# Kernel optimization log

Hardware: AMD Instinct MI355X
Metric: run time of the kernel (lower is better)

## Reference

```python
import jax, jax.numpy as jnp
import numpy as np

NUM_TOKENS = 8192
CODEBOOK_DIM = 64
BETA = 0.25
DECAY = 0.99
EPS = 1e-05
B, C, H, W = 32, 64, 32, 32


def setup_inputs() -> dict:
    key = jax.random.key(0)
    k1, k2, k3, k4 = jax.random.split(key, 4)
    z = jax.random.normal(k1, (B, C, H, W), dtype=jnp.float32)
    emb = jax.random.normal(k2, (NUM_TOKENS, CODEBOOK_DIM), dtype=jnp.float32)
    ema_w = jax.random.normal(k3, (NUM_TOKENS, CODEBOOK_DIM), dtype=jnp.float32)
    cluster_size = jax.random.uniform(k4, (NUM_TOKENS,), dtype=jnp.float32)
    return {"z": z, "emb": emb, "ema_w": ema_w, "cluster_size": cluster_size}


def reference(z, emb, ema_w, cluster_size):
    # NCHW -> NHWC, flatten to [N, D]
    z_nhwc = jnp.transpose(z, (0, 2, 3, 1))
    z_flat = z_nhwc.reshape(-1, CODEBOOK_DIM)  # [N, D]

    # squared distances: ||z||^2 + ||e||^2 - 2 z e^T  -> [N, K]
    d = (jnp.sum(z_flat * z_flat, axis=1, keepdims=True)
         + jnp.sum(emb * emb, axis=1)
         - 2.0 * jnp.einsum('nd,kd->nk', z_flat, emb))
    idx = jnp.argmin(d, axis=1)  # [N] int

    z_q = emb[idx].reshape(z_nhwc.shape)  # gather + reshape

    # EMA updates (training-mode buffer math); one-hot matmuls expressed as segment sums
    new_cluster = jax.ops.segment_sum(jnp.ones_like(idx, dtype=z.dtype), idx, num_segments=NUM_TOKENS)
    cs = DECAY * cluster_size + (1.0 - DECAY) * new_cluster
    new_ema_w = jax.ops.segment_sum(z_flat, idx, num_segments=NUM_TOKENS)
    ema_w_out = DECAY * ema_w + (1.0 - DECAY) * new_ema_w
    cs_sum = jnp.sum(cs)
    cs_norm = (cs + EPS) / (cs_sum + NUM_TOKENS * EPS)
    emb_out = ema_w_out / cs_norm[:, None]

    # commitment loss uses z_q from the OLD codebook (as in torch code)
    loss = BETA * jnp.mean((jax.lax.stop_gradient(z_q) - z_nhwc) ** 2)

    # straight-through estimator, back to NCHW
    z_q_st = z_nhwc + jax.lax.stop_gradient(z_q - z_nhwc)
    z_q_st = jnp.transpose(z_q_st, (0, 3, 1, 2))
    return z_q_st, loss, idx, cs_norm, ema_w_out, emb_out
```

## Files before the change

kernel.cpp:

```cpp
#include <hip/hip_runtime.h>
#include <float.h>

#define N_TOK   32768
#define DIM     64
#define K_CODES 8192
#define HWSZ    1024
#define CHW     65536
#define NELEM   2097152

typedef short  bf16x8 __attribute__((ext_vector_type(8)));
typedef float  f32x16 __attribute__((ext_vector_type(16)));

static __device__ __forceinline__ unsigned short f2bf(float x) {
    unsigned u = __float_as_uint(x);
    unsigned r = u + 0x7FFFu + ((u >> 16) & 1u);
    return (unsigned short)(r >> 16);
}
static __device__ __forceinline__ float bf2f(unsigned short h) {
    return __uint_as_float(((unsigned)h) << 16);
}

__global__ __launch_bounds__(256) void prep_e(const float* __restrict__ emb,
                                              unsigned short* __restrict__ blob,
                                              float* __restrict__ eng,
                                              unsigned long long* __restrict__ packed,
                                              int* __restrict__ cnt_i,
                                              float* __restrict__ sums) {
    __shared__ float part[512];
    const int gid = blockIdx.x * 256 + threadIdx.x;
    packed[gid] = ~0ull;
    if (gid < K_CODES) cnt_i[gid] = 0;
    if (gid < 2) sums[gid] = 0.f;

    int tile = blockIdx.x;
    #pragma unroll
    for (int u0 = 0; u0 < 2; ++u0) {
        int u = threadIdx.x + u0 * 256;
        int s = u >> 7, h = (u >> 6) & 1, n = u & 63;
        const float* src = emb + (tile * 64 + n) * 64 + s * 16 + h * 8;
        float4 v0 = *(const float4*)src;
        float4 v1 = *(const float4*)(src + 4);
        float x[8] = {v0.x, v0.y, v0.z, v0.w, v1.x, v1.y, v1.z, v1.w};
        unsigned short hi[8], lo[8];
        float ss = 0.f;
        #pragma unroll
        for (int j = 0; j < 8; ++j) {
            hi[j] = f2bf(x[j]);
            lo[j] = f2bf(x[j] - bf2f(hi[j]));
            ss += x[j] * x[j];
        }
        part[u] = ss;
        unsigned short* dhi = blob + (size_t)tile * 8192 + ((s * 2 + 0) * 2 + h) * 512 + n * 8;
        unsigned short* dlo = blob + (size_t)tile * 8192 + ((s * 2 + 1) * 2 + h) * 512 + n * 8;
        uint4 ph, pl;
        ph.x = (unsigned)hi[0] | ((unsigned)hi[1] << 16);
        ph.y = (unsigned)hi[2] | ((unsigned)hi[3] << 16);
        ph.z = (unsigned)hi[4] | ((unsigned)hi[5] << 16);
        ph.w = (unsigned)hi[6] | ((unsigned)hi[7] << 16);
        pl.x = (unsigned)lo[0] | ((unsigned)lo[1] << 16);
        pl.y = (unsigned)lo[2] | ((unsigned)lo[3] << 16);
        pl.z = (unsigned)lo[4] | ((unsigned)lo[5] << 16);
        pl.w = (unsigned)lo[6] | ((unsigned)lo[7] << 16);
        *(uint4*)dhi = ph;
        *(uint4*)dlo = pl;
    }
    __syncthreads();
    if (threadIdx.x < 64) {
        float s = 0.f;
        #pragma unroll
        for (int j = 0; j < 8; ++j) s += part[threadIdx.x + j * 64];
        eng[tile * 64 + threadIdx.x] = s;
    }
}

static __device__ __forceinline__ void loadB(const unsigned short* __restrict__ base,
                                             int h, bf16x8* Bh, bf16x8* Bl) {
    #pragma unroll
    for (int s = 0; s < 4; ++s) {
        Bh[s] = *(const bf16x8*)(base + (4 * s + h) * 512);
        Bl[s] = *(const bf16x8*)(base + (4 * s + 2 + h) * 512);
    }
}

__global__ __launch_bounds__(256, 2) void vq_argmin(const float* __restrict__ z,
                                                    const unsigned short* __restrict__ blob,
                                                    const float* __restrict__ eng,
                                                    unsigned long long* __restrict__ packed) {
    __shared__ __align__(16) unsigned short zh[128 * 72];
    __shared__ __align__(16) unsigned short zl[128 * 72];
    __shared__ unsigned long long red[256];

    const int tid  = threadIdx.x;
    const int lane = tid & 63;
    const int wid  = tid >> 6;
    const int wr   = wid >> 1, wc = wid & 1;
    const int l31  = lane & 31, h = lane >> 5;

    const int tb = blockIdx.x & 255;
    const int ks = blockIdx.x >> 8;
    const int n0 = tb * 128;
    const int zbase = (n0 >> 10) * CHW + (n0 & 1023);
    const int t0 = ks * 64, t1 = t0 + 64;
    const int wcb = (wc * 32 + l31) * 8;
    const int colb = wc * 32 + l31;

    {
        int f4 = tid & 31;
        int c0 = tid >> 5;
        #pragma unroll
        for (int r = 0; r < 8; ++r) {
            int c = c0 * 8 + r;
            float4 v = *(const float4*)(z + zbase + c * HWSZ + f4 * 4);
            float x[4] = {v.x, v.y, v.z, v.w};
            #pragma unroll
            for (int e = 0; e < 4; ++e) {
                int t = f4 * 4 + e;
                unsigned short hi = f2bf(x[e]);
                zh[t * 72 + c] = hi;
                zl[t * 72 + c] = f2bf(x[e] - bf2f(hi));
            }
        }
    }

    bf16x8 B0h[4], B0l[4], B1h[4], B1l[4];
    float engv0, engv1;
    loadB(blob + (size_t)t0 * 8192 + wcb, h, B0h, B0l);
    engv0 = eng[t0 * 64 + colb];

    __syncthreads();

    bf16x8 Af[2][4][2];
    #pragma unroll
    for (int mt = 0; mt < 2; ++mt) {
        int row = wr * 64 + mt * 32 + l31;
        #pragma unroll
        for (int s = 0; s < 4; ++s) {
            Af[mt][s][0] = *(const bf16x8*)(&zh[row * 72 + s * 16 + h * 8]);
            Af[mt][s][1] = *(const bf16x8*)(&zl[row * 72 + s * 16 + h * 8]);
        }
    }

    float minv0[16], minv1[16];
    int   mini0[16], mini1[16];
    #pragma unroll
    for (int r = 0; r < 16; ++r) {
        minv0[r] = FLT_MAX; minv1[r] = FLT_MAX;
        mini0[r] = 0;       mini1[r] = 0;
    }

    #define COMPUTE(KT, BH, BL, ENGV)                                                  \
    {                                                                                  \
        f32x16 ac0, ac1;                                                               \
        _Pragma("unroll")                                                              \
        for (int r = 0; r < 16; ++r) { ac0[r] = 0.f; ac1[r] = 0.f; }                   \
        _Pragma("unroll")                                                              \
        for (int s = 0; s < 4; ++s) {                                                  \
            ac0 = __builtin_amdgcn_mfma_f32_32x32x16_bf16(Af[0][s][1], BH[s], ac0, 0, 0, 0); \
            ac1 = __builtin_amdgcn_mfma_f32_32x32x16_bf16(Af[1][s][1], BH[s], ac1, 0, 0, 0); \
            ac0 = __builtin_amdgcn_mfma_f32_32x32x16_bf16(Af[0][s][0], BL[s], ac0, 0, 0, 0); \
            ac1 = __builtin_amdgcn_mfma_f32_32x32x16_bf16(Af[1][s][0], BL[s], ac1, 0, 0, 0); \
            ac0 = __builtin_amdgcn_mfma_f32_32x32x16_bf16(Af[0][s][0], BH[s], ac0, 0, 0, 0); \
            ac1 = __builtin_amdgcn_mfma_f32_32x32x16_bf16(Af[1][s][0], BH[s], ac1, 0, 0, 0); \
        }                                                                              \
        const int col = (KT) * 64 + colb;                                              \
        _Pragma("unroll")                                                              \
        for (int r = 0; r < 16; ++r) {                                                 \
            float d0 = fmaf(-2.f, ac0[r], ENGV);                                       \
            if (d0 < minv0[r]) { minv0[r] = d0; mini0[r] = col; }                      \
            float d1 = fmaf(-2.f, ac1[r], ENGV);                                       \
            if (d1 < minv1[r]) { minv1[r] = d1; mini1[r] = col; }                      \
        }                                                                              \
    }

    for (int kt = t0; kt < t1; kt += 2) {
        loadB(blob + (size_t)(kt + 1) * 8192 + wcb, h, B1h, B1l);
        engv1 = eng[(kt + 1) * 64 + colb];
        COMPUTE(kt, B0h, B0l, engv0);
        if (kt + 2 < t1) {
            loadB(blob + (size_t)(kt + 2) * 8192 + wcb, h, B0h, B0l);
            engv0 = eng[(kt + 2) * 64 + colb];
        }
        COMPUTE(kt + 1, B1h, B1l, engv1);
    }
    #undef COMPUTE

    #pragma unroll
    for (int mt = 0; mt < 2; ++mt) {
        unsigned long long pv[16];
        #pragma unroll
        for (int r = 0; r < 16; ++r) {
            float v = mt ? minv1[r] : minv0[r];
            int   i = mt ? mini1[r] : mini0[r];
            unsigned u = __float_as_uint(v);
            u = (u & 0x80000000u) ? ~u : (u | 0x80000000u);
            pv[r] = ((unsigned long long)u << 32) | (unsigned)i;
        }
        #pragma unroll
        for (int m = 1; m <= 16; m <<= 1) {
            #pragma unroll
            for (int r = 0; r < 16; ++r) {
                unsigned long long o = __shfl_xor(pv[r], m, 64);
                if (o < pv[r]) pv[r] = o;
            }
        }
        #pragma unroll
        for (int r = 0; r < 16; ++r) {
            if (l31 == r) {
                int row = wr * 64 + mt * 32 + (r & 3) + 8 * (r >> 2) + 4 * h;
                red[row * 2 + wc] = pv[r];
            }
        }
    }
    __syncthreads();
    if (tid < 128) {
        unsigned long long a = red[tid * 2], b = red[tid * 2 + 1];
        unsigned long long m = (b < a) ? b : a;
        atomicMin(&packed[n0 + tid], m);
    }
}

__global__ __launch_bounds__(256) void zq_loss(const float* __restrict__ z,
                                               const float* __restrict__ emb,
                                               const float* __restrict__ ema_w,
                                               const unsigned long long* __restrict__ packed,
                                               float* __restrict__ zq_out,
                                               float* __restrict__ idx_out,
                                               int* __restrict__ idx_i32,
                                               int* __restrict__ cnt_i,
                                               float* __restrict__ loss_sum,
                                               float* __restrict__ z_t,
                                               float* __restrict__ emao_out) {
    const int tid = threadIdx.x;
    const int n0  = blockIdx.x * 64;
    const int t   = tid >> 2, q = tid & 3;
    const int n   = n0 + t;
    const int idx = (int)(packed[n] & 0xFFFFFFFFull);
    if (q == 0) {
        idx_out[n] = (float)idx;
        idx_i32[n] = idx;
        atomicAdd(&cnt_i[idx], 1);
    }
    {
        int g = blockIdx.x * 256 + tid;
        #pragma unroll
        for (int j = 0; j < 4; ++j) {
            int i = g + j * 131072;
            emao_out[i] = 0.99f * ema_w[i];
        }
    }
    const int b = n >> 10, hw = n & 1023;
    const float* er = emb + idx * 64 + q * 16;
    float4 e0 = *(const float4*)er, e1 = *(const float4*)(er + 4);
    float4 e2 = *(const float4*)(er + 8), e3 = *(const float4*)(er + 12);
    float ev[16] = {e0.x, e0.y, e0.z, e0.w, e1.x, e1.y, e1.z, e1.w,
                    e2.x, e2.y, e2.z, e2.w, e3.x, e3.y, e3.z, e3.w};
    float lsum = 0.f;
    #pragma unroll
    for (int j = 0; j < 16; ++j) {
        int c = q * 16 + j;
        float zv = z[b * CHW + c * HWSZ + hw];
        float dd = ev[j] - zv;
        zq_out[b * CHW + c * HWSZ + hw] = zv + dd;
        if (z_t) z_t[n * 64 + c] = zv;
        lsum += dd * dd;
    }
    #pragma unroll
    for (int m = 32; m >= 1; m >>= 1) lsum += __shfl_xor(lsum, m, 64);
    if ((tid & 63) == 0) atomicAdd(loss_sum, lsum);
}

__global__ __launch_bounds__(1024) void scan_cs(const int* __restrict__ cnt_i,
                                                const float* __restrict__ csize,
                                                const float* __restrict__ loss_sum,
                                                int* __restrict__ cursor,
                                                float* __restrict__ csn_out,
                                                float* __restrict__ loss_out) {
    __shared__ int   sc[1024];
    __shared__ float sf[1024];
    const int tid = threadIdx.x;
    int v[8], part = 0;
    float cv[8], fpart = 0.f;
    #pragma unroll
    for (int j = 0; j < 8; ++j) { v[j] = cnt_i[tid * 8 + j]; part += v[j]; }
    #pragma unroll
    for (int j = 0; j < 8; ++j) {
        cv[j] = 0.99f * csize[tid * 8 + j] + 0.01f * (float)v[j];
        fpart += cv[j];
    }
    sc[tid] = part;
    sf[tid] = fpart;
    __syncthreads();
    for (int off = 1; off < 1024; off <<= 1) {
        int add = (tid >= off) ? sc[tid - off] : 0;
        __syncthreads();
        sc[tid] += add;
        __syncthreads();
    }
    int run = sc[tid] - part;
    #pragma unroll
    for (int j = 0; j < 8; ++j) {
        cursor[tid * 8 + j] = run;
        run += v[j];
    }
    for (int off = 512; off >= 1; off >>= 1) {
        if (tid < off) sf[tid] += sf[tid + off];
        __syncthreads();
    }
    float denom = sf[0] + (float)(K_CODES * 1e-5);
    #pragma unroll
    for (int j = 0; j < 8; ++j) csn_out[tid * 8 + j] = (cv[j] + 1e-5f) / denom;
    if (tid == 0) *loss_out = 0.25f * (*loss_sum) * (1.0f / (float)NELEM);
}

__global__ __launch_bounds__(256) void scatter_kernel(const int* __restrict__ idx_i32,
                                                      int* __restrict__ cursor,
                                                      int* __restrict__ tok_of,
                                                      int* __restrict__ code_of) {
    int t = blockIdx.x * 256 + threadIdx.x;
    int k = idx_i32[t];
    int pos = atomicAdd(&cursor[k], 1);
    tok_of[pos] = t;
    code_of[pos] = k;
}

__global__ __launch_bounds__(256) void ema_acc(const float* __restrict__ z,
                                               const float* __restrict__ z_t,
                                               const int* __restrict__ tok_of,
                                               const int* __restrict__ code_of,
                                               float* __restrict__ emao_out) {
    const int wv   = (blockIdx.x * 256 + threadIdx.x) >> 6;
    const int lane = threadIdx.x & 63;
    const int pos0 = wv * 64;
    const int tok  = tok_of[pos0 + lane];
    const int cod  = code_of[pos0 + lane];
    float acc = 0.f;
    #pragma unroll
    for (int g = 0; g < 8; ++g) {
        int tk[8], kk[8];
        #pragma unroll
        for (int j = 0; j < 8; ++j) {
            tk[j] = __shfl(tok, g * 8 + j, 64);
            kk[j] = __shfl(cod, g * 8 + j, 64);
        }
        float v[8];
        if (z_t) {
            #pragma unroll
            for (int j = 0; j < 8; ++j) v[j] = z_t[tk[j] * 64 + lane];
        } else {
            #pragma unroll
            for (int j = 0; j < 8; ++j)
                v[j] = z[(tk[j] >> 10) * CHW + lane * HWSZ + (tk[j] & 1023)];
        }
        int knext = (g < 7) ? __shfl(cod, g * 8 + 8, 64) : -1;
        #pragma unroll
        for (int j = 0; j < 8; ++j) {
            acc += v[j];
            int kn = (j < 7) ? kk[j + 1] : knext;
            if (kn != kk[j]) {
                atomicAdd(&emao_out[kk[j] * 64 + lane], 0.01f * acc);
                acc = 0.f;
            }
        }
    }
}

__global__ __launch_bounds__(256) void final_div(const float* __restrict__ emao_out,
                                                 const float* __restrict__ csn_out,
                                                 float* __restrict__ embo_out) {
    int g = blockIdx.x * 256 + threadIdx.x;
    embo_out[g] = emao_out[g] / csn_out[g >> 6];
}

extern "C" void kernel_launch(void* const* d_in, const int* in_sizes, int n_in,
                              void* d_out, int out_size, void* d_ws, size_t ws_size,
                              hipStream_t stream) {
    (void)in_sizes; (void)n_in; (void)out_size;
    const float* z     = (const float*)d_in[0];
    const float* emb   = (const float*)d_in[1];
    const float* ema_w = (const float*)d_in[2];
    const float* csize = (const float*)d_in[3];

    float* out      = (float*)d_out;
    float* zq_out   = out;
    float* loss_out = out + 2097152;
    float* idx_out  = out + 2097153;
    float* csn_out  = out + 2129921;
    float* emao_out = out + 2138113;
    float* embo_out = out + 2662401;

    char* wsb = (char*)d_ws;
    unsigned short*     blob    = (unsigned short*)(wsb);
    float*              eng     = (float*)(wsb + 2097152);
    unsigned long long* packed  = (unsigned long long*)(wsb + 2129920);
    int*                code_of = (int*)(wsb + 2129920);
    int*                idx_i32 = (int*)(wsb + 2392064);
    int*                cnt_i   = (int*)(wsb + 2523136);
    float*              sums    = (float*)(wsb + 2555904);
    int*                cursor  = (int*)(wsb + 2555920);
    int*                tok_of  = (int*)(wsb + 2588688);
    const size_t zt_off = 2719760;
    float* z_t = (ws_size >= zt_off + (size_t)NELEM * 4) ? (float*)(wsb + zt_off) : nullptr;

    prep_e<<<128, 256, 0, stream>>>(emb, blob, eng, packed, cnt_i, sums);
    vq_argmin<<<512, 256, 0, stream>>>(z, blob, eng, packed);
    zq_loss<<<N_TOK / 64, 256, 0, stream>>>(z, emb, ema_w, packed, zq_out, idx_out,
                                            idx_i32, cnt_i, sums + 1, z_t, emao_out);
    scan_cs<<<1, 1024, 0, stream>>>(cnt_i, csize, sums + 1, cursor, csn_out, loss_out);
    scatter_kernel<<<N_TOK / 256, 256, 0, stream>>>(idx_i32, cursor, tok_of, code_of);
    ema_acc<<<128, 256, 0, stream>>>(z, z_t, tok_of, code_of, emao_out);
    final_div<<<K_CODES * DIM / 256, 256, 0, stream>>>(emao_out, csn_out, embo_out);
}
```

Before: 233.6 us.

## Transpose argmin MFMA so codes index rows, shrinking token tile to 64

Reworks the distance/argmin kernel. Codes now sit on the MFMA M dimension and tokens on N, so each lane owns a single token column and keeps one running min instead of 32. The accumulator is seeded with the code norms and z is prescaled by -2, which folds the distance FMA into the MFMA. The block tile drops to 64 tokens and the grid doubles, with launch bounds raised to 4 blocks per SM. The explicit double-buffered B prefetch is removed, and each B fragment is now reused across only one token tile instead of two, which doubles global/L2 traffic for the codebook.

```diff
diff --git a/kernel.cpp b/kernel.cpp
--- a/kernel.cpp
+++ b/kernel.cpp
@@ -73,146 +73,101 @@
     }
 }
 
-static __device__ __forceinline__ void loadB(const unsigned short* __restrict__ base,
-                                             int h, bf16x8* Bh, bf16x8* Bl) {
-    #pragma unroll
-    for (int s = 0; s < 4; ++s) {
-        Bh[s] = *(const bf16x8*)(base + (4 * s + h) * 512);
-        Bl[s] = *(const bf16x8*)(base + (4 * s + 2 + h) * 512);
-    }
-}
-
-__global__ __launch_bounds__(256, 2) void vq_argmin(const float* __restrict__ z,
+__global__ __launch_bounds__(256, 4) void vq_argmin(const float* __restrict__ z,
                                                     const unsigned short* __restrict__ blob,
                                                     const float* __restrict__ eng,
                                                     unsigned long long* __restrict__ packed) {
-    __shared__ __align__(16) unsigned short zh[128 * 72];
-    __shared__ __align__(16) unsigned short zl[128 * 72];
-    __shared__ unsigned long long red[256];
+    __shared__ __align__(16) unsigned short zh[64 * 72];
+    __shared__ __align__(16) unsigned short zl[64 * 72];
+    __shared__ unsigned long long red[64 * 2];
 
     const int tid  = threadIdx.x;
     const int lane = tid & 63;
     const int wid  = tid >> 6;
-    const int wr   = wid >> 1, wc = wid & 1;
+    const int wr   = wid >> 1;
+    const int wc   = wid & 1;
     const int l31  = lane & 31, h = lane >> 5;
 
-    const int tb = blockIdx.x & 255;
-    const int ks = blockIdx.x >> 8;
-    const int n0 = tb * 128;
+    const int tb = blockIdx.x & 511;
+    const int ks = blockIdx.x >> 9;
+    const int n0 = tb * 64;
     const int zbase = (n0 >> 10) * CHW + (n0 & 1023);
     const int t0 = ks * 64, t1 = t0 + 64;
     const int wcb = (wc * 32 + l31) * 8;
-    const int colb = wc * 32 + l31;
 
     {
-        int f4 = tid & 31;
-        int c0 = tid >> 5;
-        #pragma unroll
-        for (int r = 0; r < 8; ++r) {
-            int c = c0 * 8 + r;
+        int f4 = tid & 15;
+        int c0 = tid >> 4;
+        #pragma unroll
+        for (int r = 0; r < 4; ++r) {
+            int c = c0 * 4 + r;
             float4 v = *(const float4*)(z + zbase + c * HWSZ + f4 * 4);
             float x[4] = {v.x, v.y, v.z, v.w};
             #pragma unroll
             for (int e = 0; e < 4; ++e) {
                 int t = f4 * 4 + e;
-                unsigned short hi = f2bf(x[e]);
+                float xs = -2.0f * x[e];
+                unsigned short hi = f2bf(xs);
                 zh[t * 72 + c] = hi;
-                zl[t * 72 + c] = f2bf(x[e] - bf2f(hi));
+                zl[t * 72 + c] = f2bf(xs - bf2f(hi));
             }
         }
     }
-
-    bf16x8 B0h[4], B0l[4], B1h[4], B1l[4];
-    float engv0, engv1;
-    loadB(blob + (size_t)t0 * 8192 + wcb, h, B0h, B0l);
-    engv0 = eng[t0 * 64 + colb];
-
     __syncthreads();
 
-    bf16x8 Af[2][4][2];
-    #pragma unroll
-    for (int mt = 0; mt < 2; ++mt) {
-        int row = wr * 64 + mt * 32 + l31;
+    bf16x8 Tf[4][2];
+    {
+        int row = wr * 32 + l31;
         #pragma unroll
         for (int s = 0; s < 4; ++s) {
-            Af[mt][s][0] = *(const bf16x8*)(&zh[row * 72 + s * 16 + h * 8]);
-            Af[mt][s][1] = *(const bf16x8*)(&zl[row * 72 + s * 16 + h * 8]);
-        }
-    }
-
-    float minv0[16], minv1[16];
-    int   mini0[16], mini1[16];
-    #pragma unroll
-    for (int r = 0; r < 16; ++r) {
-        minv0[r] = FLT_MAX; minv1[r] = FLT_MAX;
-        mini0[r] = 0;       mini1[r] = 0;
-    }
-
-    #define COMPUTE(KT, BH, BL, ENGV)                                                  \
-    {                                                                                  \
-        f32x16 ac0, ac1;                                                               \
-        _Pragma("unroll")                                                              \
-        for (int r = 0; r < 16; ++r) { ac0[r] = 0.f; ac1[r] = 0.f; }                   \
-        _Pragma("unroll")                                                              \
-        for (int s = 0; s < 4; ++s) {                                                  \
-            ac0 = __builtin_amdgcn_mfma_f32_32x32x16_bf16(Af[0][s][1], BH[s], ac0, 0, 0, 0); \
-            ac1 = __builtin_amdgcn_mfma_f32_32x32x16_bf16(Af[1][s][1], BH[s], ac1, 0, 0, 0); \
-            ac0 = __builtin_amdgcn_mfma_f32_32x32x16_bf16(Af[0][s][0], BL[s], ac0, 0, 0, 0); \
-            ac1 = __builtin_amdgcn_mfma_f32_32x32x16_bf16(Af[1][s][0], BL[s], ac1, 0, 0, 0); \
-            ac0 = __builtin_amdgcn_mfma_f32_32x32x16_bf16(Af[0][s][0], BH[s], ac0, 0, 0, 0); \
-            ac1 = __builtin_amdgcn_mfma_f32_32x32x16_bf16(Af[1][s][0], BH[s], ac1, 0, 0, 0); \
-        }                                                                              \
-        const int col = (KT) * 64 + colb;                                              \
-        _Pragma("unroll")                                                              \
-        for (int r = 0; r < 16; ++r) {                                                 \
-            float d0 = fmaf(-2.f, ac0[r], ENGV);                                       \
-            if (d0 < minv0[r]) { minv0[r] = d0; mini0[r] = col; }                      \
-            float d1 = fmaf(-2.f, ac1[r], ENGV);                                       \
-            if (d1 < minv1[r]) { minv1[r] = d1; mini1[r] = col; }                      \
-        }                                                                              \
-    }
-
-    for (int kt = t0; kt < t1; kt += 2) {
-        loadB(blob + (size_t)(kt + 1) * 8192 + wcb, h, B1h, B1l);
-        engv1 = eng[(kt + 1) * 64 + colb];
-        COMPUTE(kt, B0h, B0l, engv0);
-        if (kt + 2 < t1) {
-            loadB(blob + (size_t)(kt + 2) * 8192 + wcb, h, B0h, B0l);
-            engv0 = eng[(kt + 2) * 64 + colb];
-        }
-        COMPUTE(kt + 1, B1h, B1l, engv1);
-    }
-    #undef COMPUTE
-
-    #pragma unroll
-    for (int mt = 0; mt < 2; ++mt) {
-        unsigned long long pv[16];
+            Tf[s][0] = *(const bf16x8*)(&zh[row * 72 + s * 16 + h * 8]);
+            Tf[s][1] = *(const bf16x8*)(&zl[row * 72 + s * 16 + h * 8]);
+        }
+    }
+
+    float minv = FLT_MAX;
+    int   mini = 0;
+
+    for (int kt = t0; kt < t1; ++kt) {
+        bf16x8 Eh[4], El[4];
+        const unsigned short* base = blob + (size_t)kt * 8192 + wcb;
+        #pragma unroll
+        for (int s = 0; s < 4; ++s) {
+            Eh[s] = *(const bf16x8*)(base + (4 * s + h) * 512);
+            El[s] = *(const bf16x8*)(base + (4 * s + 2 + h) * 512);
+        }
+        const float* ebase = eng + kt * 64 + wc * 32 + 4 * h;
+        float4 e0 = *(const float4*)(ebase);
+        float4 e1 = *(const float4*)(ebase + 8);
+        float4 e2 = *(const float4*)(ebase + 16);
+        float4 e3 = *(const float4*)(ebase + 24);
+        f32x16 ac;
+        ac[0]  = e0.x; ac[1]  = e0.y; ac[2]  = e0.z; ac[3]  = e0.w;
+        ac[4]  = e1.x; ac[5]  = e1.y; ac[6]  = e1.z; ac[7]  = e1.w;
+        ac[8]  = e2.x; ac[9]  = e2.y; ac[10] = e2.z; ac[11] = e2.w;
+        ac[12] = e3.x; ac[13] = e3.y; ac[14] = e3.z; ac[15] = e3.w;
+        #pragma unroll
+        for (int s = 0; s < 4; ++s) {
+            ac = __builtin_amdgcn_mfma_f32_32x32x16_bf16(El[s], Tf[s][0], ac, 0, 0, 0);
+            ac = __builtin_amdgcn_mfma_f32_32x32x16_bf16(Eh[s], Tf[s][1], ac, 0, 0, 0);
+            ac = __builtin_amdgcn_mfma_f32_32x32x16_bf16(Eh[s], Tf[s][0], ac, 0, 0, 0);
+        }
+        const int cb = kt * 64 + wc * 32 + 4 * h;
         #pragma unroll
         for (int r = 0; r < 16; ++r) {
-            float v = mt ? minv1[r] : minv0[r];
-            int   i = mt ? mini1[r] : mini0[r];
-            unsigned u = __float_as_uint(v);
-            u = (u & 0x80000000u) ? ~u : (u | 0x80000000u);
-            pv[r] = ((unsigned long long)u << 32) | (unsigned)i;
-        }
-        #pragma unroll
-        for (int m = 1; m <= 16; m <<= 1) {
-            #pragma unroll
-            for (int r = 0; r < 16; ++r) {
-                unsigned long long o = __shfl_xor(pv[r], m, 64);
-                if (o < pv[r]) pv[r] = o;
-            }
-        }
-        #pragma unroll
-        for (int r = 0; r < 16; ++r) {
-            if (l31 == r) {
-                int row = wr * 64 + mt * 32 + (r & 3) + 8 * (r >> 2) + 4 * h;
-                red[row * 2 + wc] = pv[r];
-            }
-        }
-    }
+            int code = cb + (r & 3) + 8 * (r >> 2);
+            if (ac[r] < minv) { minv = ac[r]; mini = code; }
+        }
+    }
+
+    unsigned u = __float_as_uint(minv);
+    u = (u & 0x80000000u) ? ~u : (u | 0x80000000u);
+    unsigned long long key = ((unsigned long long)u << 32) | (unsigned)mini;
+    unsigned long long o = __shfl_xor(key, 32, 64);
+    if (o < key) key = o;
+    if (h == 0) red[(wr * 32 + l31) * 2 + wc] = key;
     __syncthreads();
-    if (tid < 128) {
+    if (tid < 64) {
         unsigned long long a = red[tid * 2], b = red[tid * 2 + 1];
         unsigned long long m = (b < a) ? b : a;
         atomicMin(&packed[n0 + tid], m);
@@ -402,7 +357,7 @@
     float* z_t = (ws_size >= zt_off + (size_t)NELEM * 4) ? (float*)(wsb + zt_off) : nullptr;
 
     prep_e<<<128, 256, 0, stream>>>(emb, blob, eng, packed, cnt_i, sums);
-    vq_argmin<<<512, 256, 0, stream>>>(z, blob, eng, packed);
+    vq_argmin<<<1024, 256, 0, stream>>>(z, blob, eng, packed);
     zq_loss<<<N_TOK / 64, 256, 0, stream>>>(z, emb, ema_w, packed, zq_out, idx_out,
                                             idx_i32, cnt_i, sums + 1, z_t, emao_out);
     scan_cs<<<1, 1024, 0, stream>>>(cnt_i, csize, sums + 1, cursor, csn_out, loss_out);
```

New measurement: 251.0 us. +7.4%, slower.
